# Kernel optimization log

Measured on AMD Instinct MI355X. Metric: run time of the kernel, lower is better.

## Reference

```python
import jax, jax.numpy as jnp
import numpy as np
from jax import lax

E = 4; D_MODEL = 128; D_FF = 128; DT_RANK = 32; D_STATE = 16
L = 12; PAD = 12  # padding_factor=1.0 -> pad L extra zeros
K_TOP = 6; U = 1e-6; EPS = 1e-5
BATCH = 8; NODES = 307; BN = BATCH * NODES
FREQ_IN = (L + PAD) // 2 + 1 + K_TOP  # 19
FREQ_OUT = L // 2 + 1                 # 7


def setup_inputs() -> dict:
    key = jax.random.key(0)
    ks = jax.random.split(key, 14)
    x = jax.random.normal(ks[0], (BN, L, D_MODEL), jnp.float32)
    graph = jax.random.normal(ks[1], (BATCH, L, D_FF, D_FF), jnp.float32) * (1.0 / D_FF)
    in_w = jax.random.normal(ks[2], (E, 2 * D_FF, D_MODEL), jnp.float32) * 0.05
    in_b = jax.random.normal(ks[3], (E, 2 * D_FF), jnp.float32) * 0.02
    x_w = jax.random.normal(ks[4], (E, DT_RANK + 2 * D_STATE + D_FF, D_FF), jnp.float32) * 0.05
    dt_w = jax.random.uniform(ks[5], (E, D_FF, DT_RANK), jnp.float32,
                              -(DT_RANK ** -0.5), DT_RANK ** -0.5)
    dt_b = -2.0 + 0.1 * jax.random.normal(ks[6], (E, D_FF), jnp.float32)
    A_log = jnp.broadcast_to(jnp.log(jnp.arange(1, D_STATE + 1, dtype=jnp.float32))[None, None, :],
                             (E, 1, D_STATE))
    out_w = jax.random.normal(ks[7], (E, D_MODEL, D_FF), jnp.float32) * 0.05
    out_b = jax.random.normal(ks[8], (E, D_MODEL), jnp.float32) * 0.02
    fw_r = jax.random.normal(ks[9], (E, FREQ_OUT, FREQ_IN), jnp.float32) * (FREQ_IN ** -0.5)
    fw_i = jax.random.normal(ks[10], (E, FREQ_OUT, FREQ_IN), jnp.float32) * (FREQ_IN ** -0.5)
    norm_w = jnp.ones((E, D_MODEL), jnp.float32)
    blk_w = jnp.full((E,), 0.5, jnp.float32)
    blk_b = jnp.full((E,), 0.5, jnp.float32)
    return dict(x=x, graph=graph, in_w=in_w, in_b=in_b, x_w=x_w, dt_w=dt_w, dt_b=dt_b,
                A_log=A_log, out_w=out_w, out_b=out_b, fw_r=fw_r, fw_i=fw_i,
                norm_w=norm_w, blk_w=blk_w, blk_b=blk_b)


def _rmsnorm(x, w):
    return x * lax.rsqrt(jnp.mean(x * x, axis=-1, keepdims=True) + EPS) * w


def _mamba_block(x, graph, in_w, in_b, x_w, dt_w, dt_b, A_log, out_w, out_b, fw_r, fw_i):
    bn, Ls, d = x.shape
    # --- FFT frequency gating ---
    x_padded = jnp.concatenate([x, jnp.zeros((bn, PAD, d), x.dtype)], axis=1)
    fp = jnp.fft.rfft(x_padded, axis=1)          # [bn, 13, d] complex
    f = jnp.fft.rfft(x, axis=1)                  # [bn, 7, d] complex
    sq_adj = (f.real + U) ** 2 + (f.imag + U) ** 2
    fs = -jnp.sort(-sq_adj, axis=1)[:, :K_TOP]   # top-K along freq dim, descending
    cat = jnp.concatenate([fp, fs.astype(fp.dtype)], axis=1)  # [bn, 19, d]
    W = lax.complex(fw_r, fw_i)                  # [7, 19]
    freq_proj = jnp.einsum('bkd,ok->bod', cat, W)  # [bn, 7, d]
    wf = jax.nn.softmax(freq_proj.real ** 2 + freq_proj.imag ** 2, axis=2)
    x_freq = jnp.fft.irfft(wf * f, axis=1)       # [bn, 12, d] (n = 2*(7-1))
    # --- input projection ---
    xz = x @ in_w.T + in_b
    xs, z = jnp.split(xz, 2, axis=-1)
    xs = jax.nn.silu(xs)
    # --- SSM ---
    A = -jnp.exp(A_log.astype(jnp.float32))      # [1, d_state]
    dbcd = xs @ x_w.T
    delta, B, C, Dp = jnp.split(dbcd, [DT_RANK, DT_RANK + D_STATE, DT_RANK + 2 * D_STATE], axis=-1)
    delta = jax.nn.softplus(delta @ dt_w.T + dt_b)  # [bn, L, d_ff]
    # graph mixing over nodes: bn = batch * n
    batch = graph.shape[0]
    delta = delta.reshape(batch, -1, Ls, D_FF)
    delta = jnp.einsum('bnsd,bsda->bnsa', delta, graph).reshape(bn, Ls, D_FF)
    deltaA = jnp.exp(delta[..., None] * A)             # [bn, L, d_ff, d_state]
    BX = delta[..., None] * B[:, :, None, :] * xs[..., None]
    dA_t = jnp.moveaxis(deltaA, 1, 0)
    bx_t = jnp.moveaxis(BX, 1, 0)

    def step(h, ab):
        dA, bx = ab
        h = dA * h + bx
        return h, h

    h0 = jnp.zeros((bn, D_FF, D_STATE), xs.dtype)
    _, hs = lax.scan(step, h0, (dA_t, bx_t))
    hs = jnp.moveaxis(hs, 0, 1)                        # [bn, L, d_ff, d_state]
    y = jnp.einsum('blds,bls->bld', hs, C) + Dp * xs
    # --- gate + output ---
    out = y * jax.nn.silu(z) * x_freq
    return out @ out_w.T + out_b


def reference(x, graph, in_w, in_b, x_w, dt_w, dt_b, A_log, out_w, out_b,
              fw_r, fw_i, norm_w, blk_w, blk_b):
    for i in range(E):
        xn = _rmsnorm(x, norm_w[i])
        out = _mamba_block(xn, graph, in_w[i], in_b[i], x_w[i], dt_w[i], dt_b[i],
                           A_log[i], out_w[i], out_b[i], fw_r[i], fw_i[i])
        out = blk_w[i] * out + blk_b[i]
        x = x + out  # dropout is identity in eval
    return jax.nn.silu(x)
```

## Files before the change

kernel.cpp:

```cpp
#include <hip/hip_runtime.h>
#include <math.h>

#define BN    2456
#define LSEQ  12
#define DM    128
#define NODES 307
#define MROWS 29472
#define FREQ_BLKS  1228
#define FUSED_BLKS 1920

typedef __bf16 bfx8 __attribute__((ext_vector_type(8)));
typedef __bf16 bfx4 __attribute__((ext_vector_type(4)));
typedef float  f32x4 __attribute__((ext_vector_type(4)));

#define MFMA16(a, b, c) __builtin_amdgcn_mfma_f32_16x16x32_bf16(a, b, c, 0, 0, 0)

__device__ __forceinline__ float fsilu(float v)     { return v / (1.0f + __expf(-v)); }
__device__ __forceinline__ float fsoftplus(float x) { return fmaxf(x, 0.f) + __logf(1.0f + __expf(-fabsf(x))); }

__global__ __launch_bounds__(256)
void k_convert(const float* __restrict__ in_w, const float* __restrict__ x_w,
               const float* __restrict__ dt_w, const float* __restrict__ out_w,
               const float* __restrict__ graph,
               const float* __restrict__ fw_r, const float* __restrict__ fw_i,
               __bf16* __restrict__ in_w_sw, __bf16* __restrict__ x_w_sw,
               __bf16* __restrict__ dtw_sw, __bf16* __restrict__ out_w_sw,
               __bf16* __restrict__ graph_sw, float* __restrict__ mw) {
    int idx = blockIdx.x * 256 + threadIdx.x;
    if (idx < 131072) {
        int o = idx;
        int e = o >> 15, r = o & 32767;
        int frag = r >> 9, lane = (r >> 3) & 63, j = r & 7;
        int nt = frag >> 2, kc = frag & 3, lm = lane & 15, lq = lane >> 4;
        in_w_sw[o] = (__bf16)in_w[e * 32768 + (nt * 16 + lm) * 128 + kc * 32 + lq * 8 + j];
        return;
    }
    idx -= 131072;
    if (idx < 98304) {
        int o = idx;
        int e = o / 24576, r = o - e * 24576;
        int frag = r >> 9, lane = (r >> 3) & 63, j = r & 7;
        int nt = frag >> 2, kc = frag & 3, lm = lane & 15, lq = lane >> 4;
        x_w_sw[o] = (__bf16)x_w[e * 24576 + (nt * 16 + lm) * 128 + kc * 32 + lq * 8 + j];
        return;
    }
    idx -= 98304;
    if (idx < 16384) {
        int o = idx;
        int e = o >> 12, r = o & 4095;
        int nt = r >> 9, lane = (r >> 3) & 63, j = r & 7;
        int lm = lane & 15, lq = lane >> 4;
        dtw_sw[o] = (__bf16)dt_w[e * 4096 + (nt * 16 + lm) * 32 + lq * 8 + j];
        return;
    }
    idx -= 16384;
    if (idx < 65536) {
        int o = idx;
        int e = o >> 14, r = o & 16383;
        int frag = r >> 9, lane = (r >> 3) & 63, j = r & 7;
        int f = frag >> 2, kc = frag & 3, lm = lane & 15, lq = lane >> 4;
        out_w_sw[o] = (__bf16)out_w[e * 16384 + (f * 16 + lm) * 128 + kc * 32 + lq * 8 + j];
        return;
    }
    idx -= 65536;
    if (idx < 1572864) {
        int bl = idx >> 14, r = idx & 16383;
        int dd = r >> 7, a = r & 127;
        int nt = a >> 4, lm = a & 15, kc = dd >> 5, lq = (dd >> 3) & 3, j = dd & 7;
        graph_sw[(size_t)bl * 16384 + ((size_t)((nt * 4 + kc) * 64 + lq * 16 + lm)) * 8 + j] =
            (__bf16)graph[(size_t)bl * 16384 + dd * 128 + a];
        return;
    }
    idx -= 1572864;
    if (idx < 336) {
        int o = idx;
        int e = o / 84, r = o - e * 84;
        int o2 = r / 12, l = r - o2 * 12;
        float mr = 0.f, mi = 0.f;
        for (int k = 0; k < 13; ++k) {
            float sv, cv;
            __sincosf(6.283185307179586f * (float)(k * l) / 24.0f, &sv, &cv);
            const float wr = fw_r[e * 133 + o2 * 19 + k], wi = fw_i[e * 133 + o2 * 19 + k];
            mr += wr * cv + wi * sv;
            mi += wi * cv - wr * sv;
        }
        mw[e * 256 + (o2 * 12 + l) * 2]     = mr;
        mw[e * 256 + (o2 * 12 + l) * 2 + 1] = mi;
        return;
    }
    idx -= 336;
    if (idx < 168) {
        int o = idx;
        int e = o / 42, r = o - e * 42;
        int o2 = r / 6, k = r - o2 * 6;
        mw[e * 256 + 168 + (o2 * 6 + k) * 2]     = fw_r[e * 133 + o2 * 19 + 13 + k];
        mw[e * 256 + 168 + (o2 * 6 + k) * 2 + 1] = fw_i[e * 133 + o2 * 19 + 13 + k];
    }
}

__global__ __launch_bounds__(256)
void k_fused(const float* __restrict__ xcur, const float* __restrict__ norm_w,
             const __bf16* __restrict__ WiSw, const float* __restrict__ in_b,
             const __bf16* __restrict__ WxSw, const __bf16* __restrict__ DWSw,
             const float* __restrict__ dt_b, const __bf16* __restrict__ GSw,
             const float* __restrict__ mw,
             __bf16* __restrict__ scanp, float* __restrict__ bcf32,
             __bf16* __restrict__ xfq_bf, int e) {
    const int tid = threadIdx.x;
    const int bid0 = blockIdx.x;
    int isFreq, wid;
    if (bid0 < 2 * FREQ_BLKS) { isFreq = !(bid0 & 1); wid = bid0 >> 1; }
    else                      { isFreq = 0; wid = FREQ_BLKS + (bid0 - 2 * FREQ_BLKS); }

    if (isFreq) {
        __shared__ float sred2[2][2][12];
        const int hh = tid >> 7, t7 = tid & 127;
        const int lane = tid & 63, w2 = (tid >> 6) & 1;
        const int row = wid * 2 + hh;
        const int b = row / NODES, n = row - b * NODES;

        constexpr float SQ32 = 0.8660254037844386f;
        constexpr float C12[12] = {1.f, SQ32, 0.5f, 0.f, -0.5f, -SQ32, -1.f, -SQ32, -0.5f, 0.f, 0.5f, SQ32};
        constexpr float S12[12] = {0.f, 0.5f, SQ32, 1.f, SQ32, 0.5f, 0.f, -0.5f, -SQ32, -1.f, -SQ32, -0.5f};

        const float* xp = xcur + (size_t)row * 1536 + t7;
        float xv[12], v[12];
#pragma unroll
        for (int l = 0; l < 12; ++l) { xv[l] = xp[l * 128]; v[l] = xv[l] * xv[l]; }
#pragma unroll
        for (int off = 32; off; off >>= 1)
#pragma unroll
            for (int i = 0; i < 12; ++i) v[i] += __shfl_xor(v[i], off, 64);
        if (lane == 0) {
#pragma unroll
            for (int i = 0; i < 12; ++i) sred2[hh][w2][i] = v[i];
        }
        __syncthreads();
#pragma unroll
        for (int i = 0; i < 12; ++i) v[i] = sred2[hh][0][i] + sred2[hh][1][i];
        __syncthreads();

        const float nrmw = norm_w[e * DM + t7];
        float xnr[12];
#pragma unroll
        for (int l = 0; l < 12; ++l)
            xnr[l] = xv[l] * rsqrtf(v[l] * (1.0f / 128.0f) + 1e-5f) * nrmw;

        float fr[7], fi[7];
#pragma unroll
        for (int o2 = 0; o2 < 7; ++o2) {
            float r = 0.f, im = 0.f;
#pragma unroll
            for (int l = 0; l < 12; ++l) {
                const int t = (o2 * l) % 12;
                r += xnr[l] * C12[t];
                im -= xnr[l] * S12[t];
            }
            fr[o2] = r; fi[o2] = im;
        }

        float a7[7];
#pragma unroll
        for (int o2 = 0; o2 < 7; ++o2) {
            const float ar = fr[o2] + 1e-6f, ai = fi[o2] + 1e-6f;
            a7[o2] = ar * ar + ai * ai;
        }
#pragma unroll
        for (int pss = 0; pss < 6; ++pss)
#pragma unroll
            for (int j = 0; j < 6; ++j) {
                const float hi = fmaxf(a7[j], a7[j + 1]);
                const float lo = fminf(a7[j], a7[j + 1]);
                a7[j] = hi; a7[j + 1] = lo;
            }

        const float* Me = mw + e * 256;
        float p7[7];
#pragma unroll
        for (int o2 = 0; o2 < 7; ++o2) {
            float pr = 0.f, pi = 0.f;
#pragma unroll
            for (int l = 0; l < 12; ++l) {
                pr += xnr[l] * Me[(o2 * 12 + l) * 2];
                pi += xnr[l] * Me[(o2 * 12 + l) * 2 + 1];
            }
#pragma unroll
            for (int k = 0; k < 6; ++k) {
                pr += a7[k] * Me[168 + (o2 * 6 + k) * 2];
                pi += a7[k] * Me[168 + (o2 * 6 + k) * 2 + 1];
            }
            p7[o2] = pr * pr + pi * pi;
        }

        float m7[7];
#pragma unroll
        for (int i = 0; i < 7; ++i) m7[i] = p7[i];
#pragma unroll
        for (int off = 32; off; off >>= 1)
#pragma unroll
            for (int i = 0; i < 7; ++i) m7[i] = fmaxf(m7[i], __shfl_xor(m7[i], off, 64));
        if (lane == 0) {
#pragma unroll
            for (int i = 0; i < 7; ++i) sred2[hh][w2][i] = m7[i];
        }
        __syncthreads();
#pragma unroll
        for (int i = 0; i < 7; ++i) m7[i] = fmaxf(sred2[hh][0][i], sred2[hh][1][i]);
        __syncthreads();

        float ex[7], sm[7];
#pragma unroll
        for (int i = 0; i < 7; ++i) { ex[i] = __expf(p7[i] - m7[i]); sm[i] = ex[i]; }
#pragma unroll
        for (int off = 32; off; off >>= 1)
#pragma unroll
            for (int i = 0; i < 7; ++i) sm[i] += __shfl_xor(sm[i], off, 64);
        if (lane == 0) {
#pragma unroll
            for (int i = 0; i < 7; ++i) sred2[hh][w2][i] = sm[i];
        }
        __syncthreads();
#pragma unroll
        for (int i = 0; i < 7; ++i) sm[i] = sred2[hh][0][i] + sred2[hh][1][i];

        float gr[7], gi[7];
#pragma unroll
        for (int o2 = 0; o2 < 7; ++o2) {
            const float wf = ex[o2] / sm[o2];
            gr[o2] = wf * fr[o2];
            gi[o2] = wf * fi[o2];
        }

        const size_t xb = ((size_t)(b * 12) * NODES + n) * 128 + t7;
#pragma unroll
        for (int l = 0; l < 12; ++l) {
            float val = gr[0] + ((l & 1) ? -gr[6] : gr[6]);
#pragma unroll
            for (int o2 = 1; o2 < 6; ++o2) {
                const int t = (o2 * l) % 12;
                val += 2.0f * (gr[o2] * C12[t] - gi[o2] * S12[t]);
            }
            xfq_bf[xb + (size_t)l * (NODES * 128)] = (__bf16)(val * (1.0f / 12.0f));
        }
        return;
    }

    __shared__ __bf16 sxs[16 * 136];
    __shared__ __bf16 sdelta[16 * 136];
    __shared__ __bf16 sdel32[16 * 40];

    const int bl = wid / 20;
    const int n0 = (wid - bl * 20) * 16;
    const int wave = tid >> 6, lane = tid & 63;
    const int lm = lane & 15, lq = lane >> 4;
    const int b = bl / 12, l = bl - b * 12;
    const size_t rowbase = (size_t)bl * NODES + n0;

    const int nodeA = min(n0 + lm, NODES - 1);
    const float* xrow = xcur + ((size_t)(b * NODES + nodeA) * 12 + l) * 128 + lq * 8;
    float xv[4][8];
#pragma unroll
    for (int kc = 0; kc < 4; ++kc) {
        float4 p0 = *(const float4*)(xrow + kc * 32);
        float4 p1 = *(const float4*)(xrow + kc * 32 + 4);
        xv[kc][0] = p0.x; xv[kc][1] = p0.y; xv[kc][2] = p0.z; xv[kc][3] = p0.w;
        xv[kc][4] = p1.x; xv[kc][5] = p1.y; xv[kc][6] = p1.z; xv[kc][7] = p1.w;
    }
    float ss = 0.f;
#pragma unroll
    for (int kc = 0; kc < 4; ++kc)
#pragma unroll
        for (int j = 0; j < 8; ++j) ss += xv[kc][j] * xv[kc][j];
    ss += __shfl_xor(ss, 16, 64);
    ss += __shfl_xor(ss, 32, 64);
    const float rms = rsqrtf(ss * (1.0f / 128.0f) + 1e-5f);

    bfx8 af[4];
    const float* nwp = norm_w + e * DM + lq * 8;
#pragma unroll
    for (int kc = 0; kc < 4; ++kc) {
        float4 w0 = *(const float4*)(nwp + kc * 32);
        float4 w1 = *(const float4*)(nwp + kc * 32 + 4);
        af[kc][0] = (__bf16)(xv[kc][0] * rms * w0.x);
        af[kc][1] = (__bf16)(xv[kc][1] * rms * w0.y);
        af[kc][2] = (__bf16)(xv[kc][2] * rms * w0.z);
        af[kc][3] = (__bf16)(xv[kc][3] * rms * w0.w);
        af[kc][4] = (__bf16)(xv[kc][4] * rms * w1.x);
        af[kc][5] = (__bf16)(xv[kc][5] * rms * w1.y);
        af[kc][6] = (__bf16)(xv[kc][6] * rms * w1.z);
        af[kc][7] = (__bf16)(xv[kc][7] * rms * w1.w);
    }

    const __bf16* WxP = WxSw + (size_t)e * 24576;
    bfx8 b2[3][4];
#pragma unroll
    for (int ntl = 0; ntl < 3; ++ntl)
#pragma unroll
        for (int kc = 0; kc < 4; ++kc)
            b2[ntl][kc] = *(const bfx8*)(WxP + (((wave * 3 + ntl) * 4 + kc) * 64 + lane) * 8);

    const __bf16* WiP = WiSw + (size_t)e * 32768;
    f32x4 acc[4];
#pragma unroll
    for (int nt = 0; nt < 4; ++nt) acc[nt] = (f32x4){0.f, 0.f, 0.f, 0.f};
#pragma unroll
    for (int ntl = 0; ntl < 4; ++ntl) {
        const int nt = wave * 4 + ntl;
#pragma unroll
        for (int kc = 0; kc < 4; ++kc) {
            bfx8 bb = *(const bfx8*)(WiP + ((nt * 4 + kc) * 64 + lane) * 8);
            acc[ntl] = MFMA16(af[kc], bb, acc[ntl]);
        }
    }

    const __bf16* DWp = DWSw + (size_t)e * 4096;
    bfx8 b3[2];
#pragma unroll
    for (int ntl = 0; ntl < 2; ++ntl)
        b3[ntl] = *(const bfx8*)(DWp + ((wave * 2 + ntl) * 64 + lane) * 8);
    const __bf16* Gp = GSw + (size_t)bl * 16384;
    bfx8 b4[2][4];
#pragma unroll
    for (int ntl = 0; ntl < 2; ++ntl)
#pragma unroll
        for (int kc = 0; kc < 4; ++kc)
            b4[ntl][kc] = *(const bfx8*)(Gp + (((wave * 2 + ntl) * 4 + kc) * 64 + lane) * 8);

#pragma unroll
    for (int ntl = 0; ntl < 4; ++ntl) {
        const int col = wave * 64 + ntl * 16 + lm;
        const float bias = in_b[e * 256 + col];
#pragma unroll
        for (int r = 0; r < 4; ++r) {
            const int node = lq * 4 + r;
            const float v = fsilu(acc[ntl][r] + bias);
            const int ok = (n0 + node) < NODES;
            if (col < 128) {
                sxs[node * 136 + col] = (__bf16)v;
                if (ok) scanp[(rowbase + node) * 512 + col * 4 + 1] = (__bf16)v;
            } else if (ok) {
                scanp[(rowbase + node) * 512 + (col - 128) * 4 + 3] = (__bf16)v;
            }
        }
    }
    __syncthreads();

    bfx8 ax[4];
#pragma unroll
    for (int kc = 0; kc < 4; ++kc)
        ax[kc] = *(const bfx8*)(sxs + lm * 136 + kc * 32 + lq * 8);

    f32x4 xacc[3];
#pragma unroll
    for (int nt = 0; nt < 3; ++nt) xacc[nt] = (f32x4){0.f, 0.f, 0.f, 0.f};
#pragma unroll
    for (int ntl = 0; ntl < 3; ++ntl)
#pragma unroll
        for (int kc = 0; kc < 4; ++kc)
            xacc[ntl] = MFMA16(ax[kc], b2[ntl][kc], xacc[ntl]);

#pragma unroll
    for (int ntl = 0; ntl < 3; ++ntl) {
        const int col = (wave * 3 + ntl) * 16 + lm;
#pragma unroll
        for (int r = 0; r < 4; ++r) {
            const int node = lq * 4 + r;
            const float v = xacc[ntl][r];
            const int ok = (n0 + node) < NODES;
            if (col < 32) sdel32[node * 40 + col] = (__bf16)v;
            else if (col < 64) { if (ok) bcf32[(rowbase + node) * 32 + (col - 32)] = v; }
            else if (ok) scanp[(rowbase + node) * 512 + (col - 64) * 4 + 2] = (__bf16)v;
        }
    }
    __syncthreads();

    bfx8 ad = *(const bfx8*)(sdel32 + lm * 40 + lq * 8);
    const f32x4 z4 = {0.f, 0.f, 0.f, 0.f};
#pragma unroll
    for (int ntl = 0; ntl < 2; ++ntl) {
        f32x4 dacc = MFMA16(ad, b3[ntl], z4);
        const int col = (wave * 2 + ntl) * 16 + lm;
        const float bias = dt_b[e * 128 + col];
#pragma unroll
        for (int r = 0; r < 4; ++r) {
            const int node = lq * 4 + r;
            sdelta[node * 136 + col] = (__bf16)fsoftplus(dacc[r] + bias);
        }
    }
    __syncthreads();

    bfx8 ag[4];
#pragma unroll
    for (int kc = 0; kc < 4; ++kc)
        ag[kc] = *(const bfx8*)(sdelta + lm * 136 + kc * 32 + lq * 8);

#pragma unroll
    for (int ntl = 0; ntl < 2; ++ntl) {
        f32x4 gacc = z4;
#pragma unroll
        for (int kc = 0; kc < 4; ++kc)
            gacc = MFMA16(ag[kc], b4[ntl][kc], gacc);
        const int col = (wave * 2 + ntl) * 16 + lm;
#pragma unroll
        for (int r = 0; r < 4; ++r) {
            const int node = lq * 4 + r;
            if ((n0 + node) < NODES)
                scanp[(rowbase + node) * 512 + col * 4 + 0] = (__bf16)gacc[r];
        }
    }
}

__global__ __launch_bounds__(128)
void k_scanout(const float* __restrict__ xcur, const __bf16* __restrict__ scanp,
               const float* __restrict__ bcf32, const __bf16* __restrict__ xfq_bf,
               const float* __restrict__ A_log, const __bf16* __restrict__ WoSw,
               const float* __restrict__ out_b, const float* __restrict__ blk_w,
               const float* __restrict__ blk_b, float* __restrict__ xout, int e, int last) {
    __shared__ __bf16 s_out[16 * 136];
    const int row = blockIdx.x, tid = threadIdx.x;
    const int b = row / NODES, n = row - b * NODES;

    constexpr float LOGT[16] = {0.f, 0.6931472f, 1.0986123f, 1.3862944f, 1.6094379f, 1.7917595f,
                                1.9459101f, 2.0794415f, 2.1972246f, 2.3025851f, 2.3978953f,
                                2.4849066f, 2.5649494f, 2.6390573f, 2.7080502f, 2.7725887f};

    bfx4 sc12[12];
    const size_t sb = ((size_t)(b * 12) * NODES + n) * 512 + (size_t)tid * 4;
#pragma unroll
    for (int l = 0; l < 12; ++l)
        sc12[l] = *(const bfx4*)(scanp + sb + (size_t)l * (NODES * 512));

    __bf16 xq[12];
    const size_t xb = ((size_t)(b * 12) * NODES + n) * 128 + tid;
#pragma unroll
    for (int l = 0; l < 12; ++l)
        xq[l] = xfq_bf[xb + (size_t)l * (NODES * 128)];

    int chainOK = 1;
#pragma unroll
    for (int s = 0; s < 16; ++s)
        chainOK &= (fabsf(A_log[e * 16 + s] - LOGT[s]) < 1e-4f) ? 1 : 0;

#pragma unroll
    for (int r = 12; r < 16; ++r) s_out[r * 136 + tid] = (__bf16)0.f;

    float h[16];
#pragma unroll
    for (int j = 0; j < 16; ++j) h[j] = 0.f;

    if (chainOK) {
        float q1a[12];
#pragma unroll
        for (int l = 0; l < 12; ++l) q1a[l] = __expf(-(float)sc12[l][0]);
#pragma unroll
        for (int l = 0; l < 12; ++l) {
            const float dl = (float)sc12[l][0], xsv = (float)sc12[l][1];
            const float dlx = dl * xsv;
            const float* bc = bcf32 + ((size_t)(b * 12 + l) * NODES + n) * 32;
            const float q1 = q1a[l];
            const float q2 = q1 * q1, q4 = q2 * q2, q8 = q4 * q4;
            float pw[16];
            pw[0] = q1;        pw[1] = q2;        pw[2] = q1 * q2;    pw[3] = q4;
            pw[4] = q1 * q4;   pw[5] = q2 * q4;   pw[6] = pw[2] * q4; pw[7] = q8;
            pw[8] = q1 * q8;   pw[9] = q2 * q8;   pw[10] = pw[2] * q8; pw[11] = q4 * q8;
            pw[12] = pw[4] * q8; pw[13] = pw[5] * q8; pw[14] = pw[6] * q8; pw[15] = q8 * q8;
            float y0 = 0.f, y1 = 0.f, y2 = 0.f, y3 = 0.f;
#pragma unroll
            for (int j = 0; j < 4; ++j) {
                h[j]      = pw[j]      * h[j]      + bc[j]      * dlx;  y0 += h[j]      * bc[16 + j];
                h[j + 4]  = pw[j + 4]  * h[j + 4]  + bc[j + 4]  * dlx;  y1 += h[j + 4]  * bc[20 + j];
                h[j + 8]  = pw[j + 8]  * h[j + 8]  + bc[j + 8]  * dlx;  y2 += h[j + 8]  * bc[24 + j];
                h[j + 12] = pw[j + 12] * h[j + 12] + bc[j + 12] * dlx;  y3 += h[j + 12] * bc[28 + j];
            }
            float y = (y0 + y1) + (y2 + y3);
            y += (float)sc12[l][2] * xsv;
            const float g = y * (float)sc12[l][3] * (float)xq[l];
            s_out[l * 136 + tid] = (__bf16)g;
        }
    } else {
        float As[16];
#pragma unroll
        for (int s = 0; s < 16; ++s) As[s] = -__expf(A_log[e * 16 + s]);
#pragma unroll
        for (int l = 0; l < 12; ++l) {
            const float dl = (float)sc12[l][0], xsv = (float)sc12[l][1];
            const float dlx = dl * xsv;
            const float* bc = bcf32 + ((size_t)(b * 12 + l) * NODES + n) * 32;
            float y = 0.f;
#pragma unroll
            for (int j = 0; j < 16; ++j) {
                const float a = __expf(dl * As[j]);
                h[j] = a * h[j] + bc[j] * dlx;
                y += h[j] * bc[16 + j];
            }
            y += (float)sc12[l][2] * xsv;
            const float g = y * (float)sc12[l][3] * (float)xq[l];
            s_out[l * 136 + tid] = (__bf16)g;
        }
    }
    __syncthreads();

    const int wave = tid >> 6, lane = tid & 63;
    const int lm = lane & 15, lq = lane >> 4;
    const __bf16* Wop = WoSw + (size_t)e * 16384;
    bfx8 a[4];
#pragma unroll
    for (int kc = 0; kc < 4; ++kc)
        a[kc] = *(const bfx8*)(s_out + lm * 136 + kc * 32 + lq * 8);

    f32x4 acc[4];
#pragma unroll
    for (int nt = 0; nt < 4; ++nt) acc[nt] = (f32x4){0.f, 0.f, 0.f, 0.f};
#pragma unroll
    for (int nt = 0; nt < 4; ++nt) {
        const int f = wave * 4 + nt;
#pragma unroll
        for (int kc = 0; kc < 4; ++kc) {
            bfx8 bb = *(const bfx8*)(Wop + ((f * 4 + kc) * 64 + lane) * 8);
            acc[nt] = MFMA16(a[kc], bb, acc[nt]);
        }
    }

    const float bw = blk_w[e], bb2 = blk_b[e];
#pragma unroll
    for (int nt = 0; nt < 4; ++nt) {
        const int col = wave * 64 + nt * 16 + lm;
        const float ob = out_b[e * 128 + col];
#pragma unroll
        for (int r = 0; r < 4; ++r) {
            const int m = lq * 4 + r;
            if (m < 12) {
                const size_t gi = (size_t)row * 1536 + m * 128 + col;
                float vv = bw * (acc[nt][r] + ob) + bb2 + xcur[gi];
                if (last) vv = fsilu(vv);
                xout[gi] = vv;
            }
        }
    }
}

extern "C" void kernel_launch(void* const* d_in, const int* in_sizes, int n_in,
                              void* d_out, int out_size, void* d_ws, size_t ws_size,
                              hipStream_t stream) {
    (void)in_sizes; (void)n_in; (void)out_size; (void)ws_size;
    const float* x_in   = (const float*)d_in[0];
    const float* graph  = (const float*)d_in[1];
    const float* in_w   = (const float*)d_in[2];
    const float* in_b   = (const float*)d_in[3];
    const float* x_w    = (const float*)d_in[4];
    const float* dt_w   = (const float*)d_in[5];
    const float* dt_b   = (const float*)d_in[6];
    const float* A_log  = (const float*)d_in[7];
    const float* out_w  = (const float*)d_in[8];
    const float* out_b  = (const float*)d_in[9];
    const float* fw_r   = (const float*)d_in[10];
    const float* fw_i   = (const float*)d_in[11];
    const float* norm_w = (const float*)d_in[12];
    const float* blk_w  = (const float*)d_in[13];
    const float* blk_b  = (const float*)d_in[14];
    float* out = (float*)d_out;

    float* ws = (float*)d_ws;
    size_t o = 0;
    __bf16* in_w_sw  = (__bf16*)(ws + o); o += 131072 / 2;
    __bf16* x_w_sw   = (__bf16*)(ws + o); o += 98304 / 2;
    __bf16* dtw_sw   = (__bf16*)(ws + o); o += 16384 / 2;
    __bf16* out_w_sw = (__bf16*)(ws + o); o += 65536 / 2;
    __bf16* graph_sw = (__bf16*)(ws + o); o += 1572864 / 2;
    const size_t NE = (size_t)MROWS * 128;
    __bf16* scanp    = (__bf16*)(ws + o); o += (size_t)MROWS * 512 / 2;
    __bf16* xfq_bf   = (__bf16*)(ws + o); o += NE / 2;
    float*  bcf32    = ws + o;            o += (size_t)MROWS * 32;
    float*  mw       = ws + o;            o += 1024;

    hipLaunchKernelGGL(k_convert, dim3(7362), dim3(256), 0, stream,
                       in_w, x_w, dt_w, out_w, graph, fw_r, fw_i,
                       in_w_sw, x_w_sw, dtw_sw, out_w_sw, graph_sw, mw);

    for (int e = 0; e < 4; ++e) {
        const float* xcur = (e == 0) ? x_in : (const float*)out;
        const int last = (e == 3) ? 1 : 0;
        hipLaunchKernelGGL(k_fused, dim3(2 * FREQ_BLKS + (FUSED_BLKS - FREQ_BLKS)), dim3(256), 0, stream,
                           xcur, norm_w, in_w_sw, in_b, x_w_sw, dtw_sw, dt_b, graph_sw,
                           mw, scanp, bcf32, xfq_bf, e);
        hipLaunchKernelGGL(k_scanout, dim3(BN), dim3(128), 0, stream,
                           xcur, scanp, bcf32, xfq_bf, A_log,
                           out_w_sw, out_b, blk_w, blk_b, out, e, last);
    }
}
```

Baseline: 447.6 us.

## Give each wave its own 16-node tile across all output columns in fused kernel

The GEMM part of the fused kernel now assigns each of the four waves an independent 16-node tile (64 nodes per block), and each wave computes every output column of the in-proj, x-proj, dt-proj and graph GEMMs. Before, the four waves split columns of one shared 16-node tile. This cuts the GEMM block count from 1920 to 480 and drops the interleaving of freq and GEMM blocks, so all freq blocks now come first in the grid. Each weight fragment is fetched once per 64 nodes instead of once per 16, which reduces L2 traffic for the weights. The cost is more accumulator registers (up to 12 f32x4), more LDS, and fewer, heavier blocks, which may leave some CUs idle at the tail.

```diff
diff --git a/kernel.cpp b/kernel.cpp
--- a/kernel.cpp
+++ b/kernel.cpp
@@ -7,7 +7,7 @@
 #define NODES 307
 #define MROWS 29472
 #define FREQ_BLKS  1228
-#define FUSED_BLKS 1920
+#define FUSED2_BLKS 480
 
 typedef __bf16 bfx8 __attribute__((ext_vector_type(8)));
 typedef __bf16 bfx4 __attribute__((ext_vector_type(4)));
@@ -107,16 +107,12 @@
              __bf16* __restrict__ scanp, float* __restrict__ bcf32,
              __bf16* __restrict__ xfq_bf, int e) {
     const int tid = threadIdx.x;
-    const int bid0 = blockIdx.x;
-    int isFreq, wid;
-    if (bid0 < 2 * FREQ_BLKS) { isFreq = !(bid0 & 1); wid = bid0 >> 1; }
-    else                      { isFreq = 0; wid = FREQ_BLKS + (bid0 - 2 * FREQ_BLKS); }
-
-    if (isFreq) {
+
+    if (blockIdx.x < FREQ_BLKS) {
         __shared__ float sred2[2][2][12];
         const int hh = tid >> 7, t7 = tid & 127;
         const int lane = tid & 63, w2 = (tid >> 6) & 1;
-        const int row = wid * 2 + hh;
+        const int row = blockIdx.x * 2 + hh;
         const int b = row / NODES, n = row - b * NODES;
 
         constexpr float SQ32 = 0.8660254037844386f;
@@ -245,19 +241,24 @@
         return;
     }
 
-    __shared__ __bf16 sxs[16 * 136];
-    __shared__ __bf16 sdelta[16 * 136];
-    __shared__ __bf16 sdel32[16 * 40];
-
-    const int bl = wid / 20;
-    const int n0 = (wid - bl * 20) * 16;
+    __shared__ __bf16 sxs[4 * 16 * 136];
+    __shared__ __bf16 sdelta[4 * 16 * 136];
+    __shared__ __bf16 sdel32[4 * 16 * 40];
+
+    const int fid = blockIdx.x - FREQ_BLKS;
+    const int bl = fid / 5;
+    const int n0 = (fid - bl * 5) * 64;
     const int wave = tid >> 6, lane = tid & 63;
     const int lm = lane & 15, lq = lane >> 4;
     const int b = bl / 12, l = bl - b * 12;
-    const size_t rowbase = (size_t)bl * NODES + n0;
-
-    const int nodeA = min(n0 + lm, NODES - 1);
-    const float* xrow = xcur + ((size_t)(b * NODES + nodeA) * 12 + l) * 128 + lq * 8;
+    const int nbase = n0 + wave * 16;
+    const size_t rowbase = (size_t)bl * NODES + nbase;
+    __bf16* sxsW = sxs + wave * 16 * 136;
+    __bf16* sdeltaW = sdelta + wave * 16 * 136;
+    __bf16* sdel32W = sdel32 + wave * 16 * 40;
+
+    const int ng = min(nbase + lm, NODES - 1);
+    const float* xrow = xcur + ((size_t)(b * NODES + ng) * 12 + l) * 128 + lq * 8;
     float xv[4][8];
 #pragma unroll
     for (int kc = 0; kc < 4; ++kc) {
@@ -291,121 +292,133 @@
         af[kc][7] = (__bf16)(xv[kc][7] * rms * w1.w);
     }
 
-    const __bf16* WxP = WxSw + (size_t)e * 24576;
-    bfx8 b2[3][4];
-#pragma unroll
-    for (int ntl = 0; ntl < 3; ++ntl)
+    const __bf16* WiP = WiSw + (size_t)e * 32768;
+    const f32x4 z4 = {0.f, 0.f, 0.f, 0.f};
+
+    {
+        f32x4 acc8[8];
+#pragma unroll
+        for (int ntl = 0; ntl < 8; ++ntl) acc8[ntl] = z4;
+#pragma unroll
+        for (int ntl = 0; ntl < 8; ++ntl)
+#pragma unroll
+            for (int kc = 0; kc < 4; ++kc) {
+                bfx8 bb = *(const bfx8*)(WiP + ((ntl * 4 + kc) * 64 + lane) * 8);
+                acc8[ntl] = MFMA16(af[kc], bb, acc8[ntl]);
+            }
+#pragma unroll
+        for (int ntl = 0; ntl < 8; ++ntl) {
+            const int col = ntl * 16 + lm;
+            const float bias = in_b[e * 256 + col];
+#pragma unroll
+            for (int r = 0; r < 4; ++r) {
+                const int nl = lq * 4 + r;
+                const float v = fsilu(acc8[ntl][r] + bias);
+                sxsW[nl * 136 + col] = (__bf16)v;
+                if (nbase + nl < NODES)
+                    scanp[(rowbase + nl) * 512 + col * 4 + 1] = (__bf16)v;
+            }
+        }
+    }
+    {
+        f32x4 acc8[8];
+#pragma unroll
+        for (int ntl = 0; ntl < 8; ++ntl) acc8[ntl] = z4;
+#pragma unroll
+        for (int ntl = 0; ntl < 8; ++ntl)
+#pragma unroll
+            for (int kc = 0; kc < 4; ++kc) {
+                bfx8 bb = *(const bfx8*)(WiP + (((ntl + 8) * 4 + kc) * 64 + lane) * 8);
+                acc8[ntl] = MFMA16(af[kc], bb, acc8[ntl]);
+            }
+#pragma unroll
+        for (int ntl = 0; ntl < 8; ++ntl) {
+            const int col = (ntl + 8) * 16 + lm;
+            const float bias = in_b[e * 256 + col];
+#pragma unroll
+            for (int r = 0; r < 4; ++r) {
+                const int nl = lq * 4 + r;
+                const float v = fsilu(acc8[ntl][r] + bias);
+                if (nbase + nl < NODES)
+                    scanp[(rowbase + nl) * 512 + (col - 128) * 4 + 3] = (__bf16)v;
+            }
+        }
+    }
+    __syncthreads();
+
+    {
+        bfx8 ax[4];
 #pragma unroll
         for (int kc = 0; kc < 4; ++kc)
-            b2[ntl][kc] = *(const bfx8*)(WxP + (((wave * 3 + ntl) * 4 + kc) * 64 + lane) * 8);
-
-    const __bf16* WiP = WiSw + (size_t)e * 32768;
-    f32x4 acc[4];
-#pragma unroll
-    for (int nt = 0; nt < 4; ++nt) acc[nt] = (f32x4){0.f, 0.f, 0.f, 0.f};
-#pragma unroll
-    for (int ntl = 0; ntl < 4; ++ntl) {
-        const int nt = wave * 4 + ntl;
-#pragma unroll
-        for (int kc = 0; kc < 4; ++kc) {
-            bfx8 bb = *(const bfx8*)(WiP + ((nt * 4 + kc) * 64 + lane) * 8);
-            acc[ntl] = MFMA16(af[kc], bb, acc[ntl]);
-        }
-    }
-
-    const __bf16* DWp = DWSw + (size_t)e * 4096;
-    bfx8 b3[2];
-#pragma unroll
-    for (int ntl = 0; ntl < 2; ++ntl)
-        b3[ntl] = *(const bfx8*)(DWp + ((wave * 2 + ntl) * 64 + lane) * 8);
-    const __bf16* Gp = GSw + (size_t)bl * 16384;
-    bfx8 b4[2][4];
-#pragma unroll
-    for (int ntl = 0; ntl < 2; ++ntl)
+            ax[kc] = *(const bfx8*)(sxsW + lm * 136 + kc * 32 + lq * 8);
+
+        const __bf16* WxP = WxSw + (size_t)e * 24576;
+        f32x4 acc12[12];
+#pragma unroll
+        for (int ntl = 0; ntl < 12; ++ntl) acc12[ntl] = z4;
+#pragma unroll
+        for (int ntl = 0; ntl < 12; ++ntl)
+#pragma unroll
+            for (int kc = 0; kc < 4; ++kc) {
+                bfx8 bb = *(const bfx8*)(WxP + ((ntl * 4 + kc) * 64 + lane) * 8);
+                acc12[ntl] = MFMA16(ax[kc], bb, acc12[ntl]);
+            }
+#pragma unroll
+        for (int ntl = 0; ntl < 12; ++ntl) {
+            const int col = ntl * 16 + lm;
+#pragma unroll
+            for (int r = 0; r < 4; ++r) {
+                const int nl = lq * 4 + r;
+                const float v = acc12[ntl][r];
+                const int ok = (nbase + nl) < NODES;
+                if (col < 32) sdel32W[nl * 40 + col] = (__bf16)v;
+                else if (col < 64) { if (ok) bcf32[(rowbase + nl) * 32 + (col - 32)] = v; }
+                else if (ok) scanp[(rowbase + nl) * 512 + (col - 64) * 4 + 2] = (__bf16)v;
+            }
+        }
+    }
+    __syncthreads();
+
+    {
+        bfx8 ad = *(const bfx8*)(sdel32W + lm * 40 + lq * 8);
+        const __bf16* DWp = DWSw + (size_t)e * 4096;
+#pragma unroll
+        for (int ntl = 0; ntl < 8; ++ntl) {
+            bfx8 bb = *(const bfx8*)(DWp + (ntl * 64 + lane) * 8);
+            f32x4 dacc = MFMA16(ad, bb, z4);
+            const int col = ntl * 16 + lm;
+            const float bias = dt_b[e * 128 + col];
+#pragma unroll
+            for (int r = 0; r < 4; ++r) {
+                const int nl = lq * 4 + r;
+                sdeltaW[nl * 136 + col] = (__bf16)fsoftplus(dacc[r] + bias);
+            }
+        }
+    }
+    __syncthreads();
+
+    {
+        bfx8 ag[4];
 #pragma unroll
         for (int kc = 0; kc < 4; ++kc)
-            b4[ntl][kc] = *(const bfx8*)(Gp + (((wave * 2 + ntl) * 4 + kc) * 64 + lane) * 8);
-
-#pragma unroll
-    for (int ntl = 0; ntl < 4; ++ntl) {
-        const int col = wave * 64 + ntl * 16 + lm;
-        const float bias = in_b[e * 256 + col];
-#pragma unroll
-        for (int r = 0; r < 4; ++r) {
-            const int node = lq * 4 + r;
-            const float v = fsilu(acc[ntl][r] + bias);
-            const int ok = (n0 + node) < NODES;
-            if (col < 128) {
-                sxs[node * 136 + col] = (__bf16)v;
-                if (ok) scanp[(rowbase + node) * 512 + col * 4 + 1] = (__bf16)v;
-            } else if (ok) {
-                scanp[(rowbase + node) * 512 + (col - 128) * 4 + 3] = (__bf16)v;
-            }
-        }
-    }
-    __syncthreads();
-
-    bfx8 ax[4];
-#pragma unroll
-    for (int kc = 0; kc < 4; ++kc)
-        ax[kc] = *(const bfx8*)(sxs + lm * 136 + kc * 32 + lq * 8);
-
-    f32x4 xacc[3];
-#pragma unroll
-    for (int nt = 0; nt < 3; ++nt) xacc[nt] = (f32x4){0.f, 0.f, 0.f, 0.f};
-#pragma unroll
-    for (int ntl = 0; ntl < 3; ++ntl)
-#pragma unroll
-        for (int kc = 0; kc < 4; ++kc)
-            xacc[ntl] = MFMA16(ax[kc], b2[ntl][kc], xacc[ntl]);
-
-#pragma unroll
-    for (int ntl = 0; ntl < 3; ++ntl) {
-        const int col = (wave * 3 + ntl) * 16 + lm;
-#pragma unroll
-        for (int r = 0; r < 4; ++r) {
-            const int node = lq * 4 + r;
-            const float v = xacc[ntl][r];
-            const int ok = (n0 + node) < NODES;
-            if (col < 32) sdel32[node * 40 + col] = (__bf16)v;
-            else if (col < 64) { if (ok) bcf32[(rowbase + node) * 32 + (col - 32)] = v; }
-            else if (ok) scanp[(rowbase + node) * 512 + (col - 64) * 4 + 2] = (__bf16)v;
-        }
-    }
-    __syncthreads();
-
-    bfx8 ad = *(const bfx8*)(sdel32 + lm * 40 + lq * 8);
-    const f32x4 z4 = {0.f, 0.f, 0.f, 0.f};
-#pragma unroll
-    for (int ntl = 0; ntl < 2; ++ntl) {
-        f32x4 dacc = MFMA16(ad, b3[ntl], z4);
-        const int col = (wave * 2 + ntl) * 16 + lm;
-        const float bias = dt_b[e * 128 + col];
-#pragma unroll
-        for (int r = 0; r < 4; ++r) {
-            const int node = lq * 4 + r;
-            sdelta[node * 136 + col] = (__bf16)fsoftplus(dacc[r] + bias);
-        }
-    }
-    __syncthreads();
-
-    bfx8 ag[4];
-#pragma unroll
-    for (int kc = 0; kc < 4; ++kc)
-        ag[kc] = *(const bfx8*)(sdelta + lm * 136 + kc * 32 + lq * 8);
-
-#pragma unroll
-    for (int ntl = 0; ntl < 2; ++ntl) {
-        f32x4 gacc = z4;
-#pragma unroll
-        for (int kc = 0; kc < 4; ++kc)
-            gacc = MFMA16(ag[kc], b4[ntl][kc], gacc);
-        const int col = (wave * 2 + ntl) * 16 + lm;
-#pragma unroll
-        for (int r = 0; r < 4; ++r) {
-            const int node = lq * 4 + r;
-            if ((n0 + node) < NODES)
-                scanp[(rowbase + node) * 512 + col * 4 + 0] = (__bf16)gacc[r];
+            ag[kc] = *(const bfx8*)(sdeltaW + lm * 136 + kc * 32 + lq * 8);
+
+        const __bf16* Gp = GSw + (size_t)bl * 16384;
+#pragma unroll
+        for (int ntl = 0; ntl < 8; ++ntl) {
+            f32x4 gacc = z4;
+#pragma unroll
+            for (int kc = 0; kc < 4; ++kc) {
+                bfx8 bb = *(const bfx8*)(Gp + ((ntl * 4 + kc) * 64 + lane) * 8);
+                gacc = MFMA16(ag[kc], bb, gacc);
+            }
+            const int col = ntl * 16 + lm;
+#pragma unroll
+            for (int r = 0; r < 4; ++r) {
+                const int nl = lq * 4 + r;
+                if (nbase + nl < NODES)
+                    scanp[(rowbase + nl) * 512 + col * 4 + 0] = (__bf16)gacc[r];
+            }
         }
     }
 }
@@ -580,7 +593,7 @@
     for (int e = 0; e < 4; ++e) {
         const float* xcur = (e == 0) ? x_in : (const float*)out;
         const int last = (e == 3) ? 1 : 0;
-        hipLaunchKernelGGL(k_fused, dim3(2 * FREQ_BLKS + (FUSED_BLKS - FREQ_BLKS)), dim3(256), 0, stream,
+        hipLaunchKernelGGL(k_fused, dim3(FREQ_BLKS + FUSED2_BLKS), dim3(256), 0, stream,
                            xcur, norm_w, in_w_sw, in_b, x_w_sw, dtw_sw, dt_b, graph_sw,
                            mw, scanp, bcf32, xfq_bf, e);
         hipLaunchKernelGGL(k_scanout, dim3(BN), dim3(128), 0, stream,
```

Result: faster. 429.8 us (-4.0%).
